# Performance work log

Measured on AMD Instinct MI355X. Metric: run time of the kernel, lower is better.

The kernel has to match this reference:

```python
import jax, jax.numpy as jnp
import numpy as np

NOPE, ROPE, LORA, VDIM = 128, 64, 512, 128
H, T = 16, 2048
SCALE = 1.0 / float(np.sqrt(NOPE + ROPE))  # 192**-0.5


def setup_inputs() -> dict:
    key = jax.random.key(0)
    k1, k2, k3, k4, k5 = jax.random.split(key, 5)
    return {
        "query": jax.random.normal(k1, (T, H, NOPE + ROPE), jnp.float32),
        "k_c_normed": jax.random.normal(k2, (T, LORA), jnp.float32),
        "k_pe": jax.random.normal(k3, (T, ROPE), jnp.float32),
        "w_kv_b": jax.random.normal(k4, (LORA, H * (NOPE + VDIM)), jnp.float32) * 0.02,
        "w_uv": jax.random.normal(k5, (H, LORA, VDIM), jnp.float32) * 0.02,
    }


def reference(query, k_c_normed, k_pe, w_kv_b, w_uv):
    # Causal (fresh-token, "compute friendly") MLA path of HPUUnifiedMLAImpl.
    t = query.shape[0]
    # kv_b_proj: latent -> per-head [nope | v]; only k_nope is used for scoring
    kv_nope = (k_c_normed @ w_kv_b).reshape(t, H, NOPE + VDIM)
    k_nope = kv_nope[..., :NOPE]                                   # [T,H,128]
    # k = cat(k_nope, broadcast k_pe) -> [T,H,192]
    k = jnp.concatenate(
        [k_nope, jnp.broadcast_to(k_pe[:, None, :], (t, H, ROPE))], axis=-1)
    # causal attention scores [H,T,T]
    scores = jnp.einsum('thd,shd->hts', query, k) * SCALE
    mask = jnp.tril(jnp.ones((t, t), dtype=bool))                  # causal
    scores = jnp.where(mask[None], scores, jnp.finfo(scores.dtype).min)
    p = jax.nn.softmax(scores, axis=-1)
    # value is the latent k_c, shared across heads (v_causal_latent expand)
    out_latent = jnp.einsum('hts,sl->thl', p, k_c_normed)          # [T,H,512]
    # W_UV projects latent attn output -> full v dim
    out = jnp.einsum('thl,hlv->thv', out_latent, w_uv)             # [T,H,128]
    return out.reshape(t, H * VDIM)
```

## Files before the change

### kernel.cpp

```cpp
#include <hip/hip_runtime.h>
#include <hip/hip_bf16.h>
#include <math.h>

#define T_SEQ 2048
#define NHEAD 16
#define DQK 192
#define DNOPE 128
#define DROPE 64
#define LORA_D 512
#define VDIM 128
#define SCALE_F 0.072168783648703216f
#define KC 32

typedef short bf16x8 __attribute__((ext_vector_type(8)));
typedef float f32x4 __attribute__((ext_vector_type(4)));

static __device__ __forceinline__ unsigned short f2bf(float x) {
  union { float f; unsigned int u; } v; v.f = x;
  unsigned int r = (v.u + 0x7fff + ((v.u >> 16) & 1)) >> 16;
  return (unsigned short)r;
}

__global__ __launch_bounds__(256) void stage_all(
    const float* __restrict__ k_c, const float* __restrict__ w_kv_b,
    const float* __restrict__ w_uv, unsigned short* __restrict__ Ab,
    unsigned short* __restrict__ BkT, unsigned short* __restrict__ BvT)
{
  __shared__ float tile[32][33];
  const int bx = blockIdx.x, role = blockIdx.y;
  const int tid = threadIdx.x;
  if (role == 0) {
    int i = (bx * 256 + tid) * 4;
    float4 v = *(const float4*)(k_c + i);
    ushort4 o = {f2bf(v.x), f2bf(v.y), f2bf(v.z), f2bf(v.w)};
    *(ushort4*)(Ab + i) = o;
    return;
  }
  const int tk = tid >> 3, tc4 = (tid & 7) * 4;
  const int wr = tid >> 3, wk4 = (tid & 7) * 4;
  if (role == 1) {
    const int k0 = (bx & 15) * 32, n0 = (bx >> 4) * 32;
    int n = n0 + tc4;
    int col = n + ((n >> 7) << 7);
    float4 v = *(const float4*)&w_kv_b[(size_t)(k0 + tk) * 4096 + col];
    tile[tk][tc4 + 0] = v.x; tile[tk][tc4 + 1] = v.y;
    tile[tk][tc4 + 2] = v.z; tile[tk][tc4 + 3] = v.w;
    __syncthreads();
    ushort4 o = {f2bf(tile[wk4 + 0][wr]), f2bf(tile[wk4 + 1][wr]),
                 f2bf(tile[wk4 + 2][wr]), f2bf(tile[wk4 + 3][wr])};
    *(ushort4*)&BkT[(size_t)(n0 + wr) * LORA_D + k0 + wk4] = o;
  } else {
    const int k0 = (bx & 15) * 32, v0 = ((bx >> 4) & 3) * 32, h = bx >> 6;
    float4 v = *(const float4*)&w_uv[(size_t)h * 65536 + (size_t)(k0 + tk) * 128 + v0 + tc4];
    tile[tk][tc4 + 0] = v.x; tile[tk][tc4 + 1] = v.y;
    tile[tk][tc4 + 2] = v.z; tile[tk][tc4 + 3] = v.w;
    __syncthreads();
    ushort4 o = {f2bf(tile[wk4 + 0][wr]), f2bf(tile[wk4 + 1][wr]),
                 f2bf(tile[wk4 + 2][wr]), f2bf(tile[wk4 + 3][wr])};
    *(ushort4*)&BvT[(size_t)(h * VDIM + v0 + wr) * LORA_D + k0 + wk4] = o;
  }
}

__global__ __launch_bounds__(256) void prep_gemm(
    const unsigned short* __restrict__ A, const unsigned short* __restrict__ BkT,
    const unsigned short* __restrict__ BvT, const float* __restrict__ k_pe,
    unsigned short* __restrict__ Kb, unsigned short* __restrict__ Vt)
{
  __shared__ unsigned short SMEM[20480];
  const int m0 = blockIdx.x * 128;
  const int by = blockIdx.y;
  const int isK = (by < 16);
  const int n0 = (isK ? by : (by - 16)) * 128;
  const unsigned short* BT = isK ? BkT : BvT;
  const int tid = threadIdx.x;
  const int wid = tid >> 6, lane = tid & 63;
  const int l16 = lane & 15, quad = lane >> 4;
  const int wm = (wid >> 1) * 64, wn = (wid & 1) * 64;
  const int srow = tid >> 2, sc = tid & 3;
  uint4 areg[2], breg[2];

  auto load_regs = [&](int k0) {
#pragma unroll
    for (int i = 0; i < 2; ++i) {
      int row = srow + i * 64;
      areg[i] = *(const uint4*)(A + (size_t)(m0 + row) * LORA_D + k0 + sc * 8);
      breg[i] = *(const uint4*)(BT + (size_t)(n0 + row) * LORA_D + k0 + sc * 8);
    }
  };
  auto store_lds = [&](int b) {
#pragma unroll
    for (int i = 0; i < 2; ++i) {
      int row = srow + i * 64;
      *(uint4*)((char*)&SMEM[b * 5120 + row * 40] + sc * 16) = areg[i];
      *(uint4*)((char*)&SMEM[10240 + b * 5120 + row * 40] + sc * 16) = breg[i];
    }
  };

  f32x4 acc[4][4];
#pragma unroll
  for (int i = 0; i < 4; ++i)
#pragma unroll
    for (int j = 0; j < 4; ++j) acc[i][j] = (f32x4){0.f, 0.f, 0.f, 0.f};

  load_regs(0);
  store_lds(0);
  __syncthreads();
  for (int kc = 0; kc < 16; ++kc) {
    const int cur = kc & 1;
    if (kc < 15) load_regs((kc + 1) * 32);
    bf16x8 af[4], bfr[4];
#pragma unroll
    for (int t = 0; t < 4; ++t) {
      af[t] = *(const bf16x8*)&SMEM[cur * 5120 + (wm + t * 16 + l16) * 40 + quad * 8];
      bfr[t] = *(const bf16x8*)&SMEM[10240 + cur * 5120 + (wn + t * 16 + l16) * 40 + quad * 8];
    }
#pragma unroll
    for (int mt = 0; mt < 4; ++mt)
#pragma unroll
      for (int nt = 0; nt < 4; ++nt)
        acc[mt][nt] = __builtin_amdgcn_mfma_f32_16x16x32_bf16(af[mt], bfr[nt], acc[mt][nt], 0, 0, 0);
    if (kc < 15) store_lds(cur ^ 1);
    __syncthreads();
  }

  unsigned short* E = SMEM;
  if (isK) {
#pragma unroll
    for (int mt = 0; mt < 4; ++mt)
#pragma unroll
      for (int nt = 0; nt < 4; ++nt) {
        int ml = wm + mt * 16 + quad * 4;
        int d = wn + nt * 16 + l16;
#pragma unroll
        for (int r = 0; r < 4; ++r)
          E[(ml + r) * 136 + d] = f2bf(acc[mt][nt][r]);
      }
  } else {
#pragma unroll
    for (int mt = 0; mt < 4; ++mt)
#pragma unroll
      for (int nt = 0; nt < 4; ++nt) {
        int ml = wm + mt * 16 + quad * 4;
        int nl = wn + nt * 16 + l16;
#pragma unroll
        for (int r = 0; r < 4; ++r)
          E[nl * 136 + ml + r] = f2bf(acc[mt][nt][r]);
      }
  }
  __syncthreads();

  if (isK) {
    const int h = by;
#pragma unroll
    for (int i = 0; i < 8; ++i) {
      int idx = (i * 256 + tid) * 8;
      int row = idx >> 7, col = idx & 127;
      uint4 v = *(const uint4*)&E[row * 136 + col];
      *(uint4*)&Kb[(size_t)h * (T_SEQ * DQK) + (size_t)(m0 + row) * DQK + col] = v;
    }
    for (int e = tid; e < 128 * 16; e += 256) {
      int row = e >> 4, c4 = (e & 15) * 4;
      float4 v = *(const float4*)&k_pe[(size_t)(m0 + row) * DROPE + c4];
      ushort4 o = {f2bf(v.x), f2bf(v.y), f2bf(v.z), f2bf(v.w)};
      *(ushort4*)&Kb[(size_t)h * (T_SEQ * DQK) + (size_t)(m0 + row) * DQK + DNOPE + c4] = o;
    }
  } else {
#pragma unroll
    for (int i = 0; i < 8; ++i) {
      int idx = (i * 256 + tid) * 8;
      int row = idx >> 7, col = idx & 127;
      uint4 v = *(const uint4*)&E[row * 136 + col];
      *(uint4*)&Vt[(size_t)(n0 + row) * T_SEQ + m0 + col] = v;
    }
  }
}

__global__ __launch_bounds__(256, 3) void flash_mfma(
    const float* __restrict__ Q, const unsigned short* __restrict__ K,
    const unsigned short* __restrict__ Vt, float* __restrict__ outp,
    float* __restrict__ Opart, float* __restrict__ Lpart, int adaptive)
{
  __shared__ unsigned short SM[2 * KC * DQK];
  __shared__ unsigned short Vsm[2 * VDIM * KC];
  __shared__ unsigned short Ps[4][16][40];
  const int id = blockIdx.x;
  const int h = ((id & 7) << 1) | ((id >> 3) & 1);
  int q0, c0, c1, slot, direct;
  if (adaptive) {
    const int b = 79 - (id >> 4);
    int j, sp, s;
    if (b < 8)       { j = b;               sp = 0;            s = 1; }
    else if (b < 24) { j = 8 + (b - 8) / 2; sp = (b - 8) % 2;  s = 2; }
    else if (b < 48) { j = 16 + (b - 24) / 3; sp = (b - 24) % 3; s = 3; }
    else             { j = 24 + (b - 48) / 4; sp = (b - 48) % 4; s = 4; }
    q0 = j * 64;
    const int n = 2 * j + 2;
    c0 = (n * sp) / s;
    c1 = (n * (sp + 1)) / s;
    direct = (s == 1);
    slot = h * 72 + (b - 8);
  } else {
    q0 = (31 - (id >> 4)) * 64;
    c0 = 0; c1 = q0 / KC + 2; direct = 1; slot = 0;
  }
  const int tid = threadIdx.x;
  const int wid = tid >> 6;
  const int lane = tid & 63;
  const int l16 = lane & 15;
  const int quad = lane >> 4;
  const int myrow = q0 + wid * 16 + quad * 4;
  const int nch = c1 - c0;

  const unsigned short* Kh = K + (size_t)h * T_SEQ * DQK;
  const unsigned short* Vth = Vt + (size_t)h * VDIM * T_SEQ;

  auto stage = [&](int buf, int s0) {
    const char* Ksrc = (const char*)(Kh + (size_t)s0 * DQK);
    char* Kdst = (char*)&SM[buf * (KC * DQK)];
#pragma unroll
    for (int i = 0; i < 3; ++i) {
      int d = tid * 16 + i * 4096;
      int row = d / 384, c = d - row * 384;
      int cs = c ^ ((row & 7) << 4);
      __builtin_amdgcn_global_load_lds(
          (const unsigned int*)(Ksrc + row * 384 + cs),
          (unsigned int*)(Kdst + d), 16, 0, 0);
    }
    const char* Vsrc = (const char*)Vth + (size_t)s0 * 2;
    char* Vdst = (char*)&Vsm[buf * (VDIM * KC)];
#pragma unroll
    for (int i = 0; i < 2; ++i) {
      int d = tid * 16 + i * 4096;
      int row = d >> 6, c = d & 63;
      int cs = c ^ ((row & 3) << 4);
      __builtin_amdgcn_global_load_lds(
          (const unsigned int*)(Vsrc + (size_t)row * (T_SEQ * 2) + cs),
          (unsigned int*)(Vdst + d), 16, 0, 0);
    }
  };

  for (int e = tid; e < 64 * 48; e += 256) {
    int row = e / 48, col = (e % 48) * 4;
    float4 q4 = *(const float4*)&Q[(size_t)(q0 + row) * (NHEAD * DQK) + h * DQK + col];
    ushort4 qp = {f2bf(q4.x), f2bf(q4.y), f2bf(q4.z), f2bf(q4.w)};
    *(ushort4*)&SM[row * DQK + col] = qp;
  }
  __syncthreads();
  bf16x8 qf[6];
#pragma unroll
  for (int ks = 0; ks < 6; ++ks)
    qf[ks] = *(const bf16x8*)&SM[(wid * 16 + l16) * DQK + ks * 32 + quad * 8];
  __syncthreads();
  stage(0, c0 * KC);
  __syncthreads();

  f32x4 oacc[8];
#pragma unroll
  for (int i = 0; i < 8; ++i) oacc[i] = (f32x4){0.f, 0.f, 0.f, 0.f};
  float lsum[4] = {0.f, 0.f, 0.f, 0.f};

  for (int ck = 0; ck < nch; ++ck) {
    const int cur = ck & 1;
    const int s0 = (c0 + ck) * KC;
    if (ck + 1 < nch) stage(cur ^ 1, s0 + KC);

    const char* Kbase = (const char*)&SM[cur * (KC * DQK)];
    f32x4 sacc[2];
    sacc[0] = (f32x4){0.f, 0.f, 0.f, 0.f};
    sacc[1] = (f32x4){0.f, 0.f, 0.f, 0.f};
    __builtin_amdgcn_s_setprio(1);
#pragma unroll
    for (int ks = 0; ks < 6; ++ks) {
      int c = ks * 64 + quad * 16;
      int r0 = l16, r1 = 16 + l16;
      bf16x8 kf0 = *(const bf16x8*)(Kbase + r0 * 384 + (c ^ ((r0 & 7) << 4)));
      bf16x8 kf1 = *(const bf16x8*)(Kbase + r1 * 384 + (c ^ ((r1 & 7) << 4)));
      sacc[0] = __builtin_amdgcn_mfma_f32_16x16x32_bf16(qf[ks], kf0, sacc[0], 0, 0, 0);
      sacc[1] = __builtin_amdgcn_mfma_f32_16x16x32_bf16(qf[ks], kf1, sacc[1], 0, 0, 0);
    }
    __builtin_amdgcn_s_setprio(0);

#pragma unroll
    for (int r = 0; r < 4; ++r) {
      int row = myrow + r;
      float p0 = (s0 + l16 <= row) ? __expf(sacc[0][r] * SCALE_F) : 0.f;
      float p1 = (s0 + 16 + l16 <= row) ? __expf(sacc[1][r] * SCALE_F) : 0.f;
      lsum[r] += p0 + p1;
      Ps[wid][quad * 4 + r][l16] = f2bf(p0);
      Ps[wid][quad * 4 + r][16 + l16] = f2bf(p1);
    }

    bf16x8 pf = *(const bf16x8*)&Ps[wid][l16][quad * 8];
    const char* Vbase = (const char*)&Vsm[cur * (VDIM * KC)];
    __builtin_amdgcn_s_setprio(1);
#pragma unroll
    for (int nt = 0; nt < 8; ++nt) {
      int vrow = nt * 16 + l16;
      bf16x8 vf = *(const bf16x8*)(Vbase + vrow * 64 + ((quad * 16) ^ ((vrow & 3) << 4)));
      oacc[nt] = __builtin_amdgcn_mfma_f32_16x16x32_bf16(pf, vf, oacc[nt], 0, 0, 0);
    }
    __builtin_amdgcn_s_setprio(0);

    __syncthreads();
  }

#pragma unroll
  for (int off = 1; off < 16; off <<= 1)
#pragma unroll
    for (int r = 0; r < 4; ++r) lsum[r] += __shfl_xor(lsum[r], off);

  if (direct) {
    float inv[4];
#pragma unroll
    for (int r = 0; r < 4; ++r) inv[r] = 1.f / lsum[r];
#pragma unroll
    for (int nt = 0; nt < 8; ++nt)
#pragma unroll
      for (int r = 0; r < 4; ++r)
        outp[(size_t)(myrow + r) * (NHEAD * VDIM) + h * VDIM + nt * 16 + l16] =
            oacc[nt][r] * inv[r];
  } else {
    const int rbase = wid * 16 + quad * 4;
#pragma unroll
    for (int nt = 0; nt < 8; ++nt)
#pragma unroll
      for (int r = 0; r < 4; ++r)
        Opart[(size_t)slot * 8192 + (rbase + r) * 128 + nt * 16 + l16] =
            oacc[nt][r];
    if (l16 == 0)
#pragma unroll
      for (int r = 0; r < 4; ++r)
        Lpart[slot * 64 + rbase + r] = lsum[r];
  }
}

__global__ __launch_bounds__(256) void reduce_out(
    const float* __restrict__ Opart, const float* __restrict__ Lpart,
    float* __restrict__ outp)
{
  const int t = blockIdx.x;
  const int h = t & 15;
  const int j = 8 + (t >> 4);
  int s, b0;
  if (j < 16)      { s = 2; b0 = 8 + (j - 8) * 2; }
  else if (j < 24) { s = 3; b0 = 24 + (j - 16) * 3; }
  else             { s = 4; b0 = 48 + (j - 24) * 4; }
  const int slot = h * 72 + (b0 - 8);
  const int q0 = j * 64;
  const int tid = threadIdx.x;
#pragma unroll
  for (int i = 0; i < 8; ++i) {
    const int f4 = tid + i * 256;
    const int row = f4 >> 5, cc = f4 & 31;
    float ax = 0.f, ay = 0.f, az = 0.f, aw = 0.f, l = 0.f;
    for (int k = 0; k < s; ++k) {
      float4 v = ((const float4*)Opart)[(size_t)(slot + k) * 2048 + f4];
      ax += v.x; ay += v.y; az += v.z; aw += v.w;
      l += Lpart[(slot + k) * 64 + row];
    }
    const float inv = 1.f / l;
    float4 o = {ax * inv, ay * inv, az * inv, aw * inv};
    ((float4*)outp)[(size_t)(q0 + row) * 512 + h * 32 + cc] = o;
  }
}

extern "C" void kernel_launch(void* const* d_in, const int* in_sizes, int n_in,
                              void* d_out, int out_size, void* d_ws, size_t ws_size,
                              hipStream_t stream) {
  const float* query  = (const float*)d_in[0];
  const float* k_c    = (const float*)d_in[1];
  const float* k_pe   = (const float*)d_in[2];
  const float* w_kv_b = (const float*)d_in[3];
  const float* w_uv   = (const float*)d_in[4];
  float* outp = (float*)d_out;

  unsigned short* Kb  = (unsigned short*)d_ws;
  unsigned short* Vt  = Kb + (size_t)NHEAD * T_SEQ * DQK;
  unsigned short* Ab  = Vt + (size_t)NHEAD * VDIM * T_SEQ;
  unsigned short* BkT = Ab + (size_t)T_SEQ * LORA_D;
  unsigned short* BvT = BkT + (size_t)2048 * LORA_D;
  float* Opart = (float*)(BvT + (size_t)2048 * LORA_D);
  float* Lpart = Opart + (size_t)16 * 72 * 64 * 128;
  const size_t need =
      (size_t)((char*)(Lpart + (size_t)16 * 72 * 64) - (char*)d_ws);
  const int adaptive = (ws_size >= need) ? 1 : 0;

  stage_all<<<dim3(1024, 3), 256, 0, stream>>>(k_c, w_kv_b, w_uv, Ab, BkT, BvT);
  prep_gemm<<<dim3(16, 32), 256, 0, stream>>>(Ab, BkT, BvT, k_pe, Kb, Vt);
  flash_mfma<<<adaptive ? 1280 : 512, 256, 0, stream>>>(query, Kb, Vt, outp,
                                                        Opart, Lpart, adaptive);
  if (adaptive)
    reduce_out<<<384, 256, 0, stream>>>(Opart, Lpart, outp);
}
```

Baseline: 195.0 us.

## Double flash query tile to 128 rows and stage prep GEMM via direct-to-LDS loads

The flash kernel now gives each wave 32 query rows (two 16-row groups), so a 128-row block reuses every K/V chunk staged in LDS for twice as many MFMAs. The adaptive split schedule, partial buffers and reduce kernel are resized to match, and the grid is halved. Separately, the prep GEMM switches from register-staged copies to global_load_lds with XOR-swizzled 64-wide K chunks, halving its loop iterations. The cost is higher register pressure in flash (twice the accumulators, with launch bounds still asking for 3 blocks per SIMD), fewer blocks to balance the load, and more LDS in prep_gemm.

```diff
diff --git a/kernel.cpp b/kernel.cpp
--- a/kernel.cpp
+++ b/kernel.cpp
@@ -66,7 +66,7 @@
     const unsigned short* __restrict__ BvT, const float* __restrict__ k_pe,
     unsigned short* __restrict__ Kb, unsigned short* __restrict__ Vt)
 {
-  __shared__ unsigned short SMEM[20480];
+  __shared__ unsigned short SMEM[32768];
   const int m0 = blockIdx.x * 128;
   const int by = blockIdx.y;
   const int isK = (by < 16);
@@ -76,25 +76,25 @@
   const int wid = tid >> 6, lane = tid & 63;
   const int l16 = lane & 15, quad = lane >> 4;
   const int wm = (wid >> 1) * 64, wn = (wid & 1) * 64;
-  const int srow = tid >> 2, sc = tid & 3;
-  uint4 areg[2], breg[2];
-
-  auto load_regs = [&](int k0) {
-#pragma unroll
-    for (int i = 0; i < 2; ++i) {
-      int row = srow + i * 64;
-      areg[i] = *(const uint4*)(A + (size_t)(m0 + row) * LORA_D + k0 + sc * 8);
-      breg[i] = *(const uint4*)(BT + (size_t)(n0 + row) * LORA_D + k0 + sc * 8);
+
+  auto stage_pg = [&](int b, int k0) {
+    const char* Asrc = (const char*)(A + (size_t)m0 * LORA_D + k0);
+    const char* Bsrc = (const char*)(BT + (size_t)n0 * LORA_D + k0);
+    char* Adst = (char*)SMEM + b * 16384;
+    char* Bdst = (char*)SMEM + 32768 + b * 16384;
+#pragma unroll
+    for (int i = 0; i < 4; ++i) {
+      int d = tid * 16 + i * 4096;
+      int row = d >> 7, c = d & 127;
+      int sc = c ^ ((row & 7) << 4);
+      __builtin_amdgcn_global_load_lds(
+          (const unsigned int*)(Asrc + (size_t)row * 1024 + sc),
+          (unsigned int*)(Adst + d), 16, 0, 0);
+      __builtin_amdgcn_global_load_lds(
+          (const unsigned int*)(Bsrc + (size_t)row * 1024 + sc),
+          (unsigned int*)(Bdst + d), 16, 0, 0);
     }
   };
-  auto store_lds = [&](int b) {
-#pragma unroll
-    for (int i = 0; i < 2; ++i) {
-      int row = srow + i * 64;
-      *(uint4*)((char*)&SMEM[b * 5120 + row * 40] + sc * 16) = areg[i];
-      *(uint4*)((char*)&SMEM[10240 + b * 5120 + row * 40] + sc * 16) = breg[i];
-    }
-  };
 
   f32x4 acc[4][4];
 #pragma unroll
@@ -102,24 +102,29 @@
 #pragma unroll
     for (int j = 0; j < 4; ++j) acc[i][j] = (f32x4){0.f, 0.f, 0.f, 0.f};
 
-  load_regs(0);
-  store_lds(0);
+  stage_pg(0, 0);
   __syncthreads();
-  for (int kc = 0; kc < 16; ++kc) {
+  for (int kc = 0; kc < 8; ++kc) {
     const int cur = kc & 1;
-    if (kc < 15) load_regs((kc + 1) * 32);
-    bf16x8 af[4], bfr[4];
-#pragma unroll
-    for (int t = 0; t < 4; ++t) {
-      af[t] = *(const bf16x8*)&SMEM[cur * 5120 + (wm + t * 16 + l16) * 40 + quad * 8];
-      bfr[t] = *(const bf16x8*)&SMEM[10240 + cur * 5120 + (wn + t * 16 + l16) * 40 + quad * 8];
-    }
-#pragma unroll
-    for (int mt = 0; mt < 4; ++mt)
-#pragma unroll
-      for (int nt = 0; nt < 4; ++nt)
-        acc[mt][nt] = __builtin_amdgcn_mfma_f32_16x16x32_bf16(af[mt], bfr[nt], acc[mt][nt], 0, 0, 0);
-    if (kc < 15) store_lds(cur ^ 1);
+    if (kc < 7) stage_pg(cur ^ 1, (kc + 1) * 64);
+#pragma unroll
+    for (int kk = 0; kk < 2; ++kk) {
+      bf16x8 af[4], bfr[4];
+#pragma unroll
+      for (int t = 0; t < 4; ++t) {
+        int ra = wm + t * 16 + l16;
+        af[t] = *(const bf16x8*)((char*)SMEM + cur * 16384 + ra * 128 +
+                                 (((kk * 4 + quad) ^ (ra & 7)) << 4));
+        int rb = wn + t * 16 + l16;
+        bfr[t] = *(const bf16x8*)((char*)SMEM + 32768 + cur * 16384 + rb * 128 +
+                                  (((kk * 4 + quad) ^ (rb & 7)) << 4));
+      }
+#pragma unroll
+      for (int mt = 0; mt < 4; ++mt)
+#pragma unroll
+        for (int nt = 0; nt < 4; ++nt)
+          acc[mt][nt] = __builtin_amdgcn_mfma_f32_16x16x32_bf16(af[mt], bfr[nt], acc[mt][nt], 0, 0, 0);
+    }
     __syncthreads();
   }
 
@@ -182,33 +187,33 @@
 {
   __shared__ unsigned short SM[2 * KC * DQK];
   __shared__ unsigned short Vsm[2 * VDIM * KC];
-  __shared__ unsigned short Ps[4][16][40];
+  __shared__ unsigned short Ps[4][32][40];
   const int id = blockIdx.x;
   const int h = ((id & 7) << 1) | ((id >> 3) & 1);
   int q0, c0, c1, slot, direct;
   if (adaptive) {
-    const int b = 79 - (id >> 4);
+    const int b = 39 - (id >> 4);
     int j, sp, s;
-    if (b < 8)       { j = b;               sp = 0;            s = 1; }
-    else if (b < 24) { j = 8 + (b - 8) / 2; sp = (b - 8) % 2;  s = 2; }
-    else if (b < 48) { j = 16 + (b - 24) / 3; sp = (b - 24) % 3; s = 3; }
-    else             { j = 24 + (b - 48) / 4; sp = (b - 48) % 4; s = 4; }
-    q0 = j * 64;
-    const int n = 2 * j + 2;
+    if (b < 4)       { j = b;                 sp = 0;            s = 1; }
+    else if (b < 12) { j = 4 + (b - 4) / 2;   sp = (b - 4) & 1;  s = 2; }
+    else if (b < 24) { j = 8 + (b - 12) / 3;  sp = (b - 12) % 3; s = 3; }
+    else             { j = 12 + (b - 24) / 4; sp = (b - 24) & 3; s = 4; }
+    q0 = j * 128;
+    const int n = 4 * j + 4;
     c0 = (n * sp) / s;
     c1 = (n * (sp + 1)) / s;
     direct = (s == 1);
-    slot = h * 72 + (b - 8);
+    slot = h * 36 + (b - 4);
   } else {
-    q0 = (31 - (id >> 4)) * 64;
-    c0 = 0; c1 = q0 / KC + 2; direct = 1; slot = 0;
+    const int j = 15 - (id >> 4);
+    q0 = j * 128; c0 = 0; c1 = 4 * j + 4; direct = 1; slot = 0;
   }
   const int tid = threadIdx.x;
   const int wid = tid >> 6;
   const int lane = tid & 63;
   const int l16 = lane & 15;
   const int quad = lane >> 4;
-  const int myrow = q0 + wid * 16 + quad * 4;
+  const int myrow = q0 + wid * 32 + quad * 4;
   const int nch = c1 - c0;
 
   const unsigned short* Kh = K + (size_t)h * T_SEQ * DQK;
@@ -239,25 +244,35 @@
     }
   };
 
-  for (int e = tid; e < 64 * 48; e += 256) {
-    int row = e / 48, col = (e % 48) * 4;
-    float4 q4 = *(const float4*)&Q[(size_t)(q0 + row) * (NHEAD * DQK) + h * DQK + col];
-    ushort4 qp = {f2bf(q4.x), f2bf(q4.y), f2bf(q4.z), f2bf(q4.w)};
-    *(ushort4*)&SM[row * DQK + col] = qp;
-  }
-  __syncthreads();
-  bf16x8 qf[6];
-#pragma unroll
-  for (int ks = 0; ks < 6; ++ks)
-    qf[ks] = *(const bf16x8*)&SM[(wid * 16 + l16) * DQK + ks * 32 + quad * 8];
-  __syncthreads();
+  bf16x8 qf[2][6];
+#pragma unroll
+  for (int p = 0; p < 2; ++p) {
+    for (int e = tid; e < 64 * 48; e += 256) {
+      int row = e / 48, col = (e % 48) * 4;
+      float4 q4 = *(const float4*)&Q[(size_t)(q0 + p * 64 + row) * (NHEAD * DQK) + h * DQK + col];
+      ushort4 qp = {f2bf(q4.x), f2bf(q4.y), f2bf(q4.z), f2bf(q4.w)};
+      *(ushort4*)&SM[row * DQK + col] = qp;
+    }
+    __syncthreads();
+    if ((wid >> 1) == p) {
+      const int lr = (wid & 1) * 32;
+#pragma unroll
+      for (int g = 0; g < 2; ++g)
+#pragma unroll
+        for (int ks = 0; ks < 6; ++ks)
+          qf[g][ks] = *(const bf16x8*)&SM[(lr + g * 16 + l16) * DQK + ks * 32 + quad * 8];
+    }
+    __syncthreads();
+  }
   stage(0, c0 * KC);
   __syncthreads();
 
-  f32x4 oacc[8];
-#pragma unroll
-  for (int i = 0; i < 8; ++i) oacc[i] = (f32x4){0.f, 0.f, 0.f, 0.f};
-  float lsum[4] = {0.f, 0.f, 0.f, 0.f};
+  f32x4 oacc[2][8];
+#pragma unroll
+  for (int g = 0; g < 2; ++g)
+#pragma unroll
+    for (int i = 0; i < 8; ++i) oacc[g][i] = (f32x4){0.f, 0.f, 0.f, 0.f};
+  float lsum[2][4] = {{0.f, 0.f, 0.f, 0.f}, {0.f, 0.f, 0.f, 0.f}};
 
   for (int ck = 0; ck < nch; ++ck) {
     const int cur = ck & 1;
@@ -265,9 +280,11 @@
     if (ck + 1 < nch) stage(cur ^ 1, s0 + KC);
 
     const char* Kbase = (const char*)&SM[cur * (KC * DQK)];
-    f32x4 sacc[2];
-    sacc[0] = (f32x4){0.f, 0.f, 0.f, 0.f};
-    sacc[1] = (f32x4){0.f, 0.f, 0.f, 0.f};
+    f32x4 sacc[2][2];
+    sacc[0][0] = (f32x4){0.f, 0.f, 0.f, 0.f};
+    sacc[0][1] = (f32x4){0.f, 0.f, 0.f, 0.f};
+    sacc[1][0] = (f32x4){0.f, 0.f, 0.f, 0.f};
+    sacc[1][1] = (f32x4){0.f, 0.f, 0.f, 0.f};
     __builtin_amdgcn_s_setprio(1);
 #pragma unroll
     for (int ks = 0; ks < 6; ++ks) {
@@ -275,29 +292,35 @@
       int r0 = l16, r1 = 16 + l16;
       bf16x8 kf0 = *(const bf16x8*)(Kbase + r0 * 384 + (c ^ ((r0 & 7) << 4)));
       bf16x8 kf1 = *(const bf16x8*)(Kbase + r1 * 384 + (c ^ ((r1 & 7) << 4)));
-      sacc[0] = __builtin_amdgcn_mfma_f32_16x16x32_bf16(qf[ks], kf0, sacc[0], 0, 0, 0);
-      sacc[1] = __builtin_amdgcn_mfma_f32_16x16x32_bf16(qf[ks], kf1, sacc[1], 0, 0, 0);
+      sacc[0][0] = __builtin_amdgcn_mfma_f32_16x16x32_bf16(qf[0][ks], kf0, sacc[0][0], 0, 0, 0);
+      sacc[0][1] = __builtin_amdgcn_mfma_f32_16x16x32_bf16(qf[0][ks], kf1, sacc[0][1], 0, 0, 0);
+      sacc[1][0] = __builtin_amdgcn_mfma_f32_16x16x32_bf16(qf[1][ks], kf0, sacc[1][0], 0, 0, 0);
+      sacc[1][1] = __builtin_amdgcn_mfma_f32_16x16x32_bf16(qf[1][ks], kf1, sacc[1][1], 0, 0, 0);
     }
     __builtin_amdgcn_s_setprio(0);
 
 #pragma unroll
-    for (int r = 0; r < 4; ++r) {
-      int row = myrow + r;
-      float p0 = (s0 + l16 <= row) ? __expf(sacc[0][r] * SCALE_F) : 0.f;
-      float p1 = (s0 + 16 + l16 <= row) ? __expf(sacc[1][r] * SCALE_F) : 0.f;
-      lsum[r] += p0 + p1;
-      Ps[wid][quad * 4 + r][l16] = f2bf(p0);
-      Ps[wid][quad * 4 + r][16 + l16] = f2bf(p1);
-    }
-
-    bf16x8 pf = *(const bf16x8*)&Ps[wid][l16][quad * 8];
+    for (int g = 0; g < 2; ++g)
+#pragma unroll
+      for (int r = 0; r < 4; ++r) {
+        int row = myrow + g * 16 + r;
+        float p0 = (s0 + l16 <= row) ? __expf(sacc[g][0][r] * SCALE_F) : 0.f;
+        float p1 = (s0 + 16 + l16 <= row) ? __expf(sacc[g][1][r] * SCALE_F) : 0.f;
+        lsum[g][r] += p0 + p1;
+        Ps[wid][g * 16 + quad * 4 + r][l16] = f2bf(p0);
+        Ps[wid][g * 16 + quad * 4 + r][16 + l16] = f2bf(p1);
+      }
+
+    bf16x8 pf0 = *(const bf16x8*)&Ps[wid][l16][quad * 8];
+    bf16x8 pf1 = *(const bf16x8*)&Ps[wid][16 + l16][quad * 8];
     const char* Vbase = (const char*)&Vsm[cur * (VDIM * KC)];
     __builtin_amdgcn_s_setprio(1);
 #pragma unroll
     for (int nt = 0; nt < 8; ++nt) {
       int vrow = nt * 16 + l16;
       bf16x8 vf = *(const bf16x8*)(Vbase + vrow * 64 + ((quad * 16) ^ ((vrow & 3) << 4)));
-      oacc[nt] = __builtin_amdgcn_mfma_f32_16x16x32_bf16(pf, vf, oacc[nt], 0, 0, 0);
+      oacc[0][nt] = __builtin_amdgcn_mfma_f32_16x16x32_bf16(pf0, vf, oacc[0][nt], 0, 0, 0);
+      oacc[1][nt] = __builtin_amdgcn_mfma_f32_16x16x32_bf16(pf1, vf, oacc[1][nt], 0, 0, 0);
     }
     __builtin_amdgcn_s_setprio(0);
 
@@ -307,30 +330,40 @@
 #pragma unroll
   for (int off = 1; off < 16; off <<= 1)
 #pragma unroll
-    for (int r = 0; r < 4; ++r) lsum[r] += __shfl_xor(lsum[r], off);
+    for (int g = 0; g < 2; ++g)
+#pragma unroll
+      for (int r = 0; r < 4; ++r) lsum[g][r] += __shfl_xor(lsum[g][r], off);
 
   if (direct) {
-    float inv[4];
-#pragma unroll
-    for (int r = 0; r < 4; ++r) inv[r] = 1.f / lsum[r];
-#pragma unroll
-    for (int nt = 0; nt < 8; ++nt)
-#pragma unroll
-      for (int r = 0; r < 4; ++r)
-        outp[(size_t)(myrow + r) * (NHEAD * VDIM) + h * VDIM + nt * 16 + l16] =
-            oacc[nt][r] * inv[r];
+    float inv[2][4];
+#pragma unroll
+    for (int g = 0; g < 2; ++g)
+#pragma unroll
+      for (int r = 0; r < 4; ++r) inv[g][r] = 1.f / lsum[g][r];
+#pragma unroll
+    for (int g = 0; g < 2; ++g)
+#pragma unroll
+      for (int nt = 0; nt < 8; ++nt)
+#pragma unroll
+        for (int r = 0; r < 4; ++r)
+          outp[(size_t)(myrow + g * 16 + r) * (NHEAD * VDIM) + h * VDIM + nt * 16 + l16] =
+              oacc[g][nt][r] * inv[g][r];
   } else {
-    const int rbase = wid * 16 + quad * 4;
-#pragma unroll
-    for (int nt = 0; nt < 8; ++nt)
-#pragma unroll
-      for (int r = 0; r < 4; ++r)
-        Opart[(size_t)slot * 8192 + (rbase + r) * 128 + nt * 16 + l16] =
-            oacc[nt][r];
+    const int rbase = wid * 32 + quad * 4;
+#pragma unroll
+    for (int g = 0; g < 2; ++g)
+#pragma unroll
+      for (int nt = 0; nt < 8; ++nt)
+#pragma unroll
+        for (int r = 0; r < 4; ++r)
+          Opart[(size_t)slot * 16384 + (rbase + g * 16 + r) * 128 + nt * 16 + l16] =
+              oacc[g][nt][r];
     if (l16 == 0)
 #pragma unroll
-      for (int r = 0; r < 4; ++r)
-        Lpart[slot * 64 + rbase + r] = lsum[r];
+      for (int g = 0; g < 2; ++g)
+#pragma unroll
+        for (int r = 0; r < 4; ++r)
+          Lpart[slot * 128 + rbase + g * 16 + r] = lsum[g][r];
   }
 }
 
@@ -340,13 +373,16 @@
 {
   const int t = blockIdx.x;
   const int h = t & 15;
-  const int j = 8 + (t >> 4);
+  const int u = t >> 4;
+  const int j = 4 + (u >> 1);
+  const int half = u & 1;
   int s, b0;
-  if (j < 16)      { s = 2; b0 = 8 + (j - 8) * 2; }
-  else if (j < 24) { s = 3; b0 = 24 + (j - 16) * 3; }
-  else             { s = 4; b0 = 48 + (j - 24) * 4; }
-  const int slot = h * 72 + (b0 - 8);
-  const int q0 = j * 64;
+  if (j < 8)       { s = 2; b0 = 4 + (j - 4) * 2; }
+  else if (j < 12) { s = 3; b0 = 12 + (j - 8) * 3; }
+  else             { s = 4; b0 = 24 + (j - 12) * 4; }
+  const int slot0 = h * 36 + (b0 - 4);
+  const int rowoff = half * 64;
+  const int q0 = j * 128 + rowoff;
   const int tid = threadIdx.x;
 #pragma unroll
   for (int i = 0; i < 8; ++i) {
@@ -354,9 +390,9 @@
     const int row = f4 >> 5, cc = f4 & 31;
     float ax = 0.f, ay = 0.f, az = 0.f, aw = 0.f, l = 0.f;
     for (int k = 0; k < s; ++k) {
-      float4 v = ((const float4*)Opart)[(size_t)(slot + k) * 2048 + f4];
+      float4 v = ((const float4*)Opart)[(size_t)(slot0 + k) * 4096 + (rowoff + row) * 32 + cc];
       ax += v.x; ay += v.y; az += v.z; aw += v.w;
-      l += Lpart[(slot + k) * 64 + row];
+      l += Lpart[(slot0 + k) * 128 + rowoff + row];
     }
     const float inv = 1.f / l;
     float4 o = {ax * inv, ay * inv, az * inv, aw * inv};
@@ -380,15 +416,15 @@
   unsigned short* BkT = Ab + (size_t)T_SEQ * LORA_D;
   unsigned short* BvT = BkT + (size_t)2048 * LORA_D;
   float* Opart = (float*)(BvT + (size_t)2048 * LORA_D);
-  float* Lpart = Opart + (size_t)16 * 72 * 64 * 128;
+  float* Lpart = Opart + (size_t)576 * 16384;
   const size_t need =
-      (size_t)((char*)(Lpart + (size_t)16 * 72 * 64) - (char*)d_ws);
+      (size_t)((char*)(Lpart + (size_t)576 * 128) - (char*)d_ws);
   const int adaptive = (ws_size >= need) ? 1 : 0;
 
   stage_all<<<dim3(1024, 3), 256, 0, stream>>>(k_c, w_kv_b, w_uv, Ab, BkT, BvT);
   prep_gemm<<<dim3(16, 32), 256, 0, stream>>>(Ab, BkT, BvT, k_pe, Kb, Vt);
-  flash_mfma<<<adaptive ? 1280 : 512, 256, 0, stream>>>(query, Kb, Vt, outp,
-                                                        Opart, Lpart, adaptive);
+  flash_mfma<<<adaptive ? 640 : 256, 256, 0, stream>>>(query, Kb, Vt, outp,
+                                                       Opart, Lpart, adaptive);
   if (adaptive)
     reduce_out<<<384, 256, 0, stream>>>(Opart, Lpart, outp);
 }
```

After: 185.9 us. 1.05x faster.

## Use direct global-to-LDS loads with XOR swizzle and larger K tiles in prep_gemm

Applied to the files above, without the earlier changes.

The prep GEMM now stages its A and B tiles with global_load_lds, which writes directly into LDS instead of passing through registers and separate LDS stores. The LDS layout changes from padded rows to an XOR-swizzled 128-byte row layout to avoid bank conflicts. The K step per iteration doubles from 32 to 64, halving the number of barriers. LDS use grows to 64KB, which may reduce occupancy, and the prep GEMM is only part of the total kernel time.

```diff
diff --git a/kernel.cpp b/kernel.cpp
--- a/kernel.cpp
+++ b/kernel.cpp
@@ -66,7 +66,7 @@
     const unsigned short* __restrict__ BvT, const float* __restrict__ k_pe,
     unsigned short* __restrict__ Kb, unsigned short* __restrict__ Vt)
 {
-  __shared__ unsigned short SMEM[20480];
+  __shared__ unsigned short SMEM[32768];
   const int m0 = blockIdx.x * 128;
   const int by = blockIdx.y;
   const int isK = (by < 16);
@@ -76,25 +76,25 @@
   const int wid = tid >> 6, lane = tid & 63;
   const int l16 = lane & 15, quad = lane >> 4;
   const int wm = (wid >> 1) * 64, wn = (wid & 1) * 64;
-  const int srow = tid >> 2, sc = tid & 3;
-  uint4 areg[2], breg[2];
-
-  auto load_regs = [&](int k0) {
-#pragma unroll
-    for (int i = 0; i < 2; ++i) {
-      int row = srow + i * 64;
-      areg[i] = *(const uint4*)(A + (size_t)(m0 + row) * LORA_D + k0 + sc * 8);
-      breg[i] = *(const uint4*)(BT + (size_t)(n0 + row) * LORA_D + k0 + sc * 8);
+
+  auto stage_pg = [&](int b, int k0) {
+    const char* Asrc = (const char*)(A + (size_t)m0 * LORA_D + k0);
+    const char* Bsrc = (const char*)(BT + (size_t)n0 * LORA_D + k0);
+    char* Adst = (char*)SMEM + b * 16384;
+    char* Bdst = (char*)SMEM + 32768 + b * 16384;
+#pragma unroll
+    for (int i = 0; i < 4; ++i) {
+      int d = tid * 16 + i * 4096;
+      int row = d >> 7, c = d & 127;
+      int sc = c ^ ((row & 7) << 4);
+      __builtin_amdgcn_global_load_lds(
+          (const unsigned int*)(Asrc + (size_t)row * 1024 + sc),
+          (unsigned int*)(Adst + d), 16, 0, 0);
+      __builtin_amdgcn_global_load_lds(
+          (const unsigned int*)(Bsrc + (size_t)row * 1024 + sc),
+          (unsigned int*)(Bdst + d), 16, 0, 0);
     }
   };
-  auto store_lds = [&](int b) {
-#pragma unroll
-    for (int i = 0; i < 2; ++i) {
-      int row = srow + i * 64;
-      *(uint4*)((char*)&SMEM[b * 5120 + row * 40] + sc * 16) = areg[i];
-      *(uint4*)((char*)&SMEM[10240 + b * 5120 + row * 40] + sc * 16) = breg[i];
-    }
-  };
 
   f32x4 acc[4][4];
 #pragma unroll
@@ -102,24 +102,29 @@
 #pragma unroll
     for (int j = 0; j < 4; ++j) acc[i][j] = (f32x4){0.f, 0.f, 0.f, 0.f};
 
-  load_regs(0);
-  store_lds(0);
-  __syncthreads();
-  for (int kc = 0; kc < 16; ++kc) {
+  stage_pg(0, 0);
+  __syncthreads();
+  for (int kc = 0; kc < 8; ++kc) {
     const int cur = kc & 1;
-    if (kc < 15) load_regs((kc + 1) * 32);
-    bf16x8 af[4], bfr[4];
-#pragma unroll
-    for (int t = 0; t < 4; ++t) {
-      af[t] = *(const bf16x8*)&SMEM[cur * 5120 + (wm + t * 16 + l16) * 40 + quad * 8];
-      bfr[t] = *(const bf16x8*)&SMEM[10240 + cur * 5120 + (wn + t * 16 + l16) * 40 + quad * 8];
-    }
-#pragma unroll
-    for (int mt = 0; mt < 4; ++mt)
-#pragma unroll
-      for (int nt = 0; nt < 4; ++nt)
-        acc[mt][nt] = __builtin_amdgcn_mfma_f32_16x16x32_bf16(af[mt], bfr[nt], acc[mt][nt], 0, 0, 0);
-    if (kc < 15) store_lds(cur ^ 1);
+    if (kc < 7) stage_pg(cur ^ 1, (kc + 1) * 64);
+#pragma unroll
+    for (int kk = 0; kk < 2; ++kk) {
+      bf16x8 af[4], bfr[4];
+#pragma unroll
+      for (int t = 0; t < 4; ++t) {
+        int ra = wm + t * 16 + l16;
+        af[t] = *(const bf16x8*)((char*)SMEM + cur * 16384 + ra * 128 +
+                                 (((kk * 4 + quad) ^ (ra & 7)) << 4));
+        int rb = wn + t * 16 + l16;
+        bfr[t] = *(const bf16x8*)((char*)SMEM + 32768 + cur * 16384 + rb * 128 +
+                                  (((kk * 4 + quad) ^ (rb & 7)) << 4));
+      }
+#pragma unroll
+      for (int mt = 0; mt < 4; ++mt)
+#pragma unroll
+        for (int nt = 0; nt < 4; ++nt)
+          acc[mt][nt] = __builtin_amdgcn_mfma_f32_16x16x32_bf16(af[mt], bfr[nt], acc[mt][nt], 0, 0, 0);
+    }
     __syncthreads();
   }
 
```

Result: faster. 170.8 us (-12.4%).
